# Kernel optimization log

Hardware: AMD Instinct MI355X
Metric: run time of the kernel (lower is better)

## Reference

```python
import jax, jax.numpy as jnp
import numpy as np
import math

SAMPLE_RATE = 44100
BASEBAND_SR = 16000
BAND_WIDTH_HZ = 8000.0
STEP_HZ = 8000.0
LOWPASS_FACTOR = 0.45
LPF_WIDTH = 6          # torchaudio resample lowpass_filter_width
ROLLOFF = 0.99         # torchaudio resample rolloff
B, T = 8, 441000


def _bands():
    nyq = SAMPLE_RATE / 2.0
    out, f = [], 0.0
    while f < nyq:
        out.append((f, min(f + BAND_WIDTH_HZ, nyq)))
        f += STEP_HZ
    return out


def _bandpass_coeffs(center, Q):
    # torchaudio bandpass_biquad, const_skirt_gain=False, normalized by a0
    w0 = 2.0 * math.pi * center / SAMPLE_RATE
    alpha = math.sin(w0) / (2.0 * Q)
    a0 = 1.0 + alpha
    b = np.array([alpha, 0.0, -alpha]) / a0
    a = np.array([1.0, -2.0 * math.cos(w0) / a0, (1.0 - alpha) / a0])
    return b, a


def _lowpass_coeffs(cutoff, Q=0.7071067811865476):
    w0 = 2.0 * math.pi * cutoff / SAMPLE_RATE
    alpha = math.sin(w0) / (2.0 * Q)
    c = math.cos(w0)
    a0 = 1.0 + alpha
    b = np.array([(1.0 - c) / 2.0, 1.0 - c, (1.0 - c) / 2.0]) / a0
    a = np.array([1.0, -2.0 * c / a0, (1.0 - alpha) / a0])
    return b, a


def _biquad(x, b0, b1, b2, a1, a2):
    # x: (..., T); coeffs broadcast against x[..., 0]. Direct-form I scan.
    xT = jnp.moveaxis(x, -1, 0)
    z = jnp.zeros_like(xT[0])
    def step(c, xt):
        x1, x2, y1, y2 = c
        y = b0 * xt + b1 * x1 + b2 * x2 - a1 * y1 - a2 * y2
        return (xt, x1, y, y1), y
    _, yT = jax.lax.scan(step, (z, z, z, z), xT)
    # torchaudio lfilter clamp=True clips final output to [-1, 1]
    return jnp.clip(jnp.moveaxis(yT, 0, -1), -1.0, 1.0)


def _resample_kernel():
    # replicates torchaudio _get_sinc_resample_kernel (sinc_interp_hann)
    g = math.gcd(SAMPLE_RATE, BASEBAND_SR)
    orig, new = SAMPLE_RATE // g, BASEBAND_SR // g  # 441, 160
    base = min(orig, new) * ROLLOFF
    width = int(math.ceil(LPF_WIDTH * orig / base))
    idx = np.arange(-width, width + orig, dtype=np.float64) / orig
    t = np.arange(0, -new, -1, dtype=np.float64)[:, None] / new + idx[None, :]
    t = np.clip(t * base, -LPF_WIDTH, LPF_WIDTH)
    window = np.cos(t * math.pi / LPF_WIDTH / 2.0) ** 2
    tp = t * math.pi
    k = np.where(tp == 0.0, 1.0, np.sin(tp) / np.where(tp == 0.0, 1.0, tp))
    k = k * window * (base / orig)
    return jnp.asarray(k[:, None, :], dtype=jnp.float32), width, orig, new


def _resample(x):
    # x: (N, T) -> (N, ceil(new*T/orig)) ; strided conv with polyphase sinc kernel
    kernel, width, orig, new = _resample_kernel()
    N, Tn = x.shape
    xp = jnp.pad(x, ((0, 0), (width, width + orig)))[:, None, :]
    y = jax.lax.conv_general_dilated(
        xp, kernel, window_strides=(orig,), padding='VALID',
        dimension_numbers=('NCH', 'OIH', 'NCH'))  # (N, new, frames)
    y = jnp.swapaxes(y, 1, 2).reshape(N, -1)
    return y[:, : int(math.ceil(new * Tn / orig))]


def _forward(x):
    # x: (B, T) -> (B, num_bands, T_baseband)
    bands = _bands()
    nb = len(bands)
    centers = np.array([0.5 * (lo + hi) for lo, hi in bands])
    Qs = np.array([max(c / (hi - lo), 0.5) for (lo, hi), c in zip(bands, centers)])
    bp = np.stack([np.concatenate(_bandpass_coeffs(c, q)) for c, q in zip(centers, Qs)])  # (nb, 6)
    bpj = jnp.asarray(bp, dtype=x.dtype)[:, :, None]  # (nb, 6, 1) -> broadcast over batch
    xb = jnp.broadcast_to(x[None], (nb,) + x.shape)   # (nb, B, T)
    # 1) per-band bandpass biquad (single batched scan over all bands)
    x_bp = _biquad(xb, bpj[:, 0], bpj[:, 1], bpj[:, 2], bpj[:, 4], bpj[:, 5])
    # 2) heterodyne mix with cosine at each band center
    t = jnp.arange(x.shape[-1], dtype=x.dtype) / SAMPLE_RATE
    cos = jnp.cos(2.0 * jnp.pi * jnp.asarray(centers, x.dtype)[:, None, None] * t[None, None, :])
    x_mix = x_bp * cos
    # 3) lowpass biquad (same coeffs for every band)
    lb, la = _lowpass_coeffs(LOWPASS_FACTOR * BASEBAND_SR)
    x_lp = _biquad(x_mix, float(lb[0]), float(lb[1]), float(lb[2]), float(la[1]), float(la[2]))
    # 4) resample 44100 -> 16000 (all bands/batch at once)
    y = _resample(x_lp.reshape(nb * x.shape[0], -1)).reshape(nb, x.shape[0], -1)
    return jnp.swapaxes(y, 0, 1)


def setup_inputs() -> dict:
    key = jax.random.key(0)
    x = jax.random.normal(key, (B, T), dtype=jnp.float32)
    return {"x": x}


def reference(x):
    return _forward(x)
```

## Files before the change

kernel.cpp:

```cpp
#include <hip/hip_runtime.h>
#include <math.h>

#define SRATE   44100
#define T_IN    441000
#define BATCH   8
#define NB      3
#define NSEQ    (NB*BATCH)
#define TB_OUT  160000
#define NEW_R   160
#define ORIG_R  441
#define KW      475
#define KP      480
#define WIDTH   17
#define NFRAMES 1000

#define LCHUNK  168
#define NCHUNK  2625
#define WARM    120

#define SCAN_BLOCKS 247
#define KT_BLOCKS   300

#define KTH_OFF 0
#define KTL_OFF (256u<<10)
#define XLP_OFF (1u<<20)

typedef __attribute__((ext_vector_type(4))) float floatx4;
typedef __attribute__((ext_vector_type(8))) short short8;

__device__ inline unsigned short f2bf(float f) {
    union { float f; unsigned u; } v; v.f = f;
    unsigned u = v.u, r = (u >> 16) & 0xffffu, rem = u & 0xffffu;
    if (rem > 0x8000u || (rem == 0x8000u && (r & 1u))) r++;
    return (unsigned short)r;
}
__device__ inline float bf2f(unsigned short h) {
    union { unsigned u; float f; } v; v.u = ((unsigned)h) << 16; return v.f;
}

__device__ inline int fragB(int p, int k) {
    int pblk = p >> 4, n = p & 15;
    int ks = k >> 5, qd = (k >> 3) & 3, j = k & 7;
    return pblk * 7680 + ks * 512 + (qd * 16 + n) * 8 + j;
}

struct ScanParams {
    float b0[NB], a1[NB], a2[NB], w[NB];
    float lb0, lb1, lb2, la1, la2;
};

__global__ __launch_bounds__(256) void scan_init_kernel(const float* __restrict__ x,
                                                        float* __restrict__ xlp,
                                                        unsigned short* __restrict__ kth,
                                                        unsigned short* __restrict__ ktl,
                                                        ScanParams P) {
    if (blockIdx.x >= SCAN_BLOCKS) {
        int idx = (blockIdx.x - SCAN_BLOCKS) * 256 + threadIdx.x;
        if (idx >= NEW_R * KP) return;
        int p = idx / KP, k = idx - p * KP;
        float v = 0.f;
        if (k < KW) {
            double t = (double)(k - WIDTH) * (158.4 / 441.0) - (double)p * 0.99;
            t = fmin(6.0, fmax(-6.0, t));
            float wc = __builtin_amdgcn_cosf((float)(t * (1.0 / 24.0)));
            double n = rint(t);
            float r2 = (float)((t - n) * 0.5);
            float sp = __builtin_amdgcn_sinf(r2 - floorf(r2));
            if (((long long)n) & 1) sp = -sp;
            float tp = (float)(t * M_PI);
            float snc = (t == 0.0) ? 1.f : sp / tp;
            v = snc * wc * wc * 0.3591836734693878f;
        }
        unsigned short h = f2bf(v);
        int flat = fragB(p, k);
        kth[flat] = h;
        ktl[flat] = f2bf(v - bf2f(h));
        return;
    }

    int id = blockIdx.x * 256 + threadIdx.x;
    if (id >= NSEQ * NCHUNK) return;
    int seq   = id / NCHUNK;
    int chunk = id - seq * NCHUNK;
    int band  = seq / BATCH;
    int batch = seq - band * BATCH;

    float b0f = (band == 0) ? P.b0[0] : (band == 1) ? P.b0[1] : P.b0[2];
    float a1f = (band == 0) ? P.a1[0] : (band == 1) ? P.a1[1] : P.a1[2];
    float a2f = (band == 0) ? P.a2[0] : (band == 1) ? P.a2[1] : P.a2[2];
    float wf  = (band == 0) ? P.w[0]  : (band == 1) ? P.w[1]  : P.w[2];
    float b2f = -b0f;
    float lb0 = P.lb0, lb1 = P.lb1, lb2 = P.lb2, la1 = P.la1, la2 = P.la2;

    const float*  xr   = x + batch * T_IN;
    float*        orow = xlp + seq * T_IN;
    const float4* xr4  = (const float4*)xr;

    int t0 = chunk * LCHUNK;
    int s0 = t0 - WARM; if (s0 < 0) s0 = 0;
    int e  = t0 + LCHUNK;
    int nq = (e - s0) >> 2;

    float bx1 = 0.f, bx2 = 0.f, by1 = 0.f, by2 = 0.f;
    float mx1 = 0.f, mx2 = 0.f, mz1 = 0.f, mz2 = 0.f;

    const float invsr  = 1.0f / 44100.0f;
    const float INV2PI = 0.15915494309189535f;
    const float PI2_A  = 6.28318548202514648f;
    const float PI2_B  = -1.7484556000744487e-7f;

    const float4 zero = make_float4(0.f, 0.f, 0.f, 0.f);
    const float4* pp = xr4 + (s0 >> 2);
    float4 c0 = pp[0];
    float4 c1 = (1 < nq) ? pp[1] : zero;
    float4 c2 = (2 < nq) ? pp[2] : zero;
    float4 c3 = (3 < nq) ? pp[3] : zero;

    for (int iq = 0; iq < nq; iq += 4) {
        float4 n0 = (iq + 4 < nq) ? pp[iq + 4] : zero;
        float4 n1 = (iq + 5 < nq) ? pp[iq + 5] : zero;
        float4 n2 = (iq + 6 < nq) ? pp[iq + 6] : zero;
        float4 n3 = (iq + 7 < nq) ? pp[iq + 7] : zero;

#define STEP(XT, TI, OUT) {                                                   \
        float y  = b0f*(XT) + b2f*bx2 - a1f*by1 - a2f*by2;                    \
        bx2 = bx1; bx1 = (XT); by2 = by1; by1 = y;                            \
        float cy = fminf(fmaxf(y, -1.f), 1.f);                                \
        float tf = (float)(TI) * invsr;                                       \
        float X  = wf * tf;                                                   \
        float kk = __builtin_rintf(X * INV2PI);                               \
        float r  = fmaf(-kk, PI2_A, X);                                       \
        r        = fmaf(-kk, PI2_B, r);                                       \
        float cv = __builtin_amdgcn_cosf(r * INV2PI);                         \
        float m  = cy * cv;                                                   \
        float z  = lb0*m + lb1*mx1 + lb2*mx2 - la1*mz1 - la2*mz2;             \
        mx2 = mx1; mx1 = m; mz2 = mz1; mz1 = z;                               \
        OUT = fminf(fmaxf(z, -1.f), 1.f); }

#define QUAD(CV, QI) {                                                        \
        int s = s0 + ((iq + QI) << 2);                                        \
        float o0, o1, o2, o3;                                                 \
        STEP(CV.x, s,     o0)                                                 \
        STEP(CV.y, s + 1, o1)                                                 \
        STEP(CV.z, s + 2, o2)                                                 \
        STEP(CV.w, s + 3, o3)                                                 \
        if (s >= t0 && s < e)                                                 \
            ((float4*)orow)[s >> 2] = make_float4(o0, o1, o2, o3); }

        QUAD(c0, 0)
        QUAD(c1, 1)
        QUAD(c2, 2)
        QUAD(c3, 3)
#undef QUAD
#undef STEP
        c0 = n0; c1 = n1; c2 = n2; c3 = n3;
    }
}

#define MT2   32

__global__ __launch_bounds__(320) void resample_mfma(const float* __restrict__ xlp,
                                                     const unsigned short* __restrict__ kth,
                                                     const unsigned short* __restrict__ ktl,
                                                     float* __restrict__ out) {
    __shared__ unsigned short Ah[2][7680];
    __shared__ unsigned short Al[2][7680];

    int bid = blockIdx.x;
    int seq = bid / MT2;
    int mt  = bid - seq * MT2;
    int band  = seq / BATCH;
    int batch = seq - band * BATCH;
    int f0 = mt * 32;
    const float* xr = xlp + seq * T_IN;

    for (int i = threadIdx.x; i < 32 * 120; i += 320) {
        int r  = i / 120;
        int q  = i - r * 120;
        int c  = q * 4;
        int fr = f0 + r;
        int base = fr * ORIG_R - WIDTH + c;
        float v0 = (base     >= 0 && base     < T_IN) ? xr[base]     : 0.f;
        float v1 = (base + 1 >= 0 && base + 1 < T_IN) ? xr[base + 1] : 0.f;
        float v2 = (base + 2 >= 0 && base + 2 < T_IN) ? xr[base + 2] : 0.f;
        float v3 = (base + 3 >= 0 && base + 3 < T_IN) ? xr[base + 3] : 0.f;
        unsigned short h0 = f2bf(v0), h1 = f2bf(v1), h2 = f2bf(v2), h3 = f2bf(v3);
        unsigned short l0 = f2bf(v0 - bf2f(h0)), l1 = f2bf(v1 - bf2f(h1));
        unsigned short l2 = f2bf(v2 - bf2f(h2)), l3 = f2bf(v3 - bf2f(h3));
        int tile = r >> 4, m = r & 15;
        int ks = c >> 5, qd = (c >> 3) & 3, j0 = c & 7;
        int slot = (qd * 16 + m) ^ ks;
        int off = ks * 512 + slot * 8 + j0;
        *(short4*)&Ah[tile][off] = make_short4(h0, h1, h2, h3);
        *(short4*)&Al[tile][off] = make_short4(l0, l1, l2, l3);
    }
    __syncthreads();

    int w    = threadIdx.x >> 6;
    int lane = threadIdx.x & 63;
    int l15  = lane & 15;
    int quad = lane >> 4;

    floatx4 acc00 = {0,0,0,0}, acc01 = {0,0,0,0};
    floatx4 acc10 = {0,0,0,0}, acc11 = {0,0,0,0};

    const unsigned short* b0h = kth + (w * 2    ) * 7680 + lane * 8;
    const unsigned short* b1h = kth + (w * 2 + 1) * 7680 + lane * 8;
    const unsigned short* b0l = ktl + (w * 2    ) * 7680 + lane * 8;
    const unsigned short* b1l = ktl + (w * 2 + 1) * 7680 + lane * 8;

#pragma unroll
    for (int ks = 0; ks < 15; ++ks) {
        int o  = ks * 512;
        int sl = o + ((lane ^ ks) << 3);
        short8 kh0 = *(const short8*)(b0h + o);
        short8 kh1 = *(const short8*)(b1h + o);
        short8 kl0 = *(const short8*)(b0l + o);
        short8 kl1 = *(const short8*)(b1l + o);
        short8 ah0 = *(const short8*)(&Ah[0][sl]);
        short8 al0 = *(const short8*)(&Al[0][sl]);
        short8 ah1 = *(const short8*)(&Ah[1][sl]);
        short8 al1 = *(const short8*)(&Al[1][sl]);

        acc00 = __builtin_amdgcn_mfma_f32_16x16x32_bf16(ah0, kh0, acc00, 0, 0, 0);
        acc00 = __builtin_amdgcn_mfma_f32_16x16x32_bf16(ah0, kl0, acc00, 0, 0, 0);
        acc00 = __builtin_amdgcn_mfma_f32_16x16x32_bf16(al0, kh0, acc00, 0, 0, 0);
        acc01 = __builtin_amdgcn_mfma_f32_16x16x32_bf16(ah0, kh1, acc01, 0, 0, 0);
        acc01 = __builtin_amdgcn_mfma_f32_16x16x32_bf16(ah0, kl1, acc01, 0, 0, 0);
        acc01 = __builtin_amdgcn_mfma_f32_16x16x32_bf16(al0, kh1, acc01, 0, 0, 0);
        acc10 = __builtin_amdgcn_mfma_f32_16x16x32_bf16(ah1, kh0, acc10, 0, 0, 0);
        acc10 = __builtin_amdgcn_mfma_f32_16x16x32_bf16(ah1, kl0, acc10, 0, 0, 0);
        acc10 = __builtin_amdgcn_mfma_f32_16x16x32_bf16(al1, kh0, acc10, 0, 0, 0);
        acc11 = __builtin_amdgcn_mfma_f32_16x16x32_bf16(ah1, kh1, acc11, 0, 0, 0);
        acc11 = __builtin_amdgcn_mfma_f32_16x16x32_bf16(ah1, kl1, acc11, 0, 0, 0);
        acc11 = __builtin_amdgcn_mfma_f32_16x16x32_bf16(al1, kh1, acc11, 0, 0, 0);
    }

    int obase = (batch * NB + band) * TB_OUT;
    int p0 = w * 32;
#pragma unroll
    for (int r = 0; r < 4; ++r) {
        int fr0 = f0 + quad * 4 + r;
        int fr1 = fr0 + 16;
        if (fr0 < NFRAMES) {
            out[obase + fr0 * NEW_R + p0 + l15]      = acc00[r];
            out[obase + fr0 * NEW_R + p0 + 16 + l15] = acc01[r];
        }
        if (fr1 < NFRAMES) {
            out[obase + fr1 * NEW_R + p0 + l15]      = acc10[r];
            out[obase + fr1 * NEW_R + p0 + 16 + l15] = acc11[r];
        }
    }
}

extern "C" void kernel_launch(void* const* d_in, const int* in_sizes, int n_in,
                              void* d_out, int out_size, void* d_ws, size_t ws_size,
                              hipStream_t stream) {
    const float*    x   = (const float*)d_in[0];
    float*          out = (float*)d_out;
    unsigned short* kth = (unsigned short*)((char*)d_ws + KTH_OFF);
    unsigned short* ktl = (unsigned short*)((char*)d_ws + KTL_OFF);
    float*          xlp = (float*)((char*)d_ws + XLP_OFF);

    ScanParams P;
    const double centers[NB] = {4000.0, 12000.0, 19025.0};
    const double Qs[NB]      = {0.5, 1.5, 19025.0 / 6050.0};
    for (int b = 0; b < NB; ++b) {
        double c  = centers[b], Q = Qs[b];
        double w0 = 2.0 * M_PI * c / 44100.0;
        double al = sin(w0) / (2.0 * Q);
        double a0 = 1.0 + al;
        P.b0[b] = (float)(al / a0);
        P.a1[b] = (float)(-2.0 * cos(w0) / a0);
        P.a2[b] = (float)((1.0 - al) / a0);
        P.w[b]  = 6.283185307179586f * (float)c;
    }
    {
        double cut = 0.45 * 16000.0;
        double Q   = 0.7071067811865476;
        double w0  = 2.0 * M_PI * cut / 44100.0;
        double al  = sin(w0) / (2.0 * Q);
        double cs  = cos(w0);
        double a0  = 1.0 + al;
        P.lb0 = (float)(((1.0 - cs) / 2.0) / a0);
        P.lb1 = (float)((1.0 - cs) / a0);
        P.lb2 = P.lb0;
        P.la1 = (float)(-2.0 * cs / a0);
        P.la2 = (float)((1.0 - al) / a0);
    }

    scan_init_kernel<<<dim3(SCAN_BLOCKS + KT_BLOCKS), dim3(256), 0, stream>>>(
        x, xlp, kth, ktl, P);

    resample_mfma<<<dim3(NSEQ * MT2), dim3(320), 0, stream>>>(xlp, kth, ktl, out);
}
```

Measured before the change: 133.1 us.

## Drop activation low-half split in resample MFMA and use 48-frame tiles

The resample kernel no longer splits the low-pass output into bf16 high and low halves. It keeps only the high half, which removes a third of the MFMAs and half of the LDS staging. Each block now covers 48 frames with three row tiles instead of 32, so fewer blocks each reuse the kernel-coefficient loads more. The clamps in the scan switch to fmed3. Activations are now held only at bf16 precision, which may weaken accuracy against the float reference.

```diff
diff --git a/kernel.cpp b/kernel.cpp
--- a/kernel.cpp
+++ b/kernel.cpp
@@ -125,7 +125,7 @@
 #define STEP(XT, TI, OUT) {                                                   \
         float y  = b0f*(XT) + b2f*bx2 - a1f*by1 - a2f*by2;                    \
         bx2 = bx1; bx1 = (XT); by2 = by1; by1 = y;                            \
-        float cy = fminf(fmaxf(y, -1.f), 1.f);                                \
+        float cy = __builtin_amdgcn_fmed3f(y, -1.f, 1.f);                     \
         float tf = (float)(TI) * invsr;                                       \
         float X  = wf * tf;                                                   \
         float kk = __builtin_rintf(X * INV2PI);                               \
@@ -135,7 +135,7 @@
         float m  = cy * cv;                                                   \
         float z  = lb0*m + lb1*mx1 + lb2*mx2 - la1*mz1 - la2*mz2;             \
         mx2 = mx1; mx1 = m; mz2 = mz1; mz1 = z;                               \
-        OUT = fminf(fmaxf(z, -1.f), 1.f); }
+        OUT = __builtin_amdgcn_fmed3f(z, -1.f, 1.f); }
 
 #define QUAD(CV, QI) {                                                        \
         int s = s0 + ((iq + QI) << 2);                                        \
@@ -157,24 +157,23 @@
     }
 }
 
-#define MT2   32
+#define MT3   21
 
 __global__ __launch_bounds__(320) void resample_mfma(const float* __restrict__ xlp,
                                                      const unsigned short* __restrict__ kth,
                                                      const unsigned short* __restrict__ ktl,
                                                      float* __restrict__ out) {
-    __shared__ unsigned short Ah[2][7680];
-    __shared__ unsigned short Al[2][7680];
+    __shared__ unsigned short Ah[3][7680];
 
     int bid = blockIdx.x;
-    int seq = bid / MT2;
-    int mt  = bid - seq * MT2;
+    int seq = bid / MT3;
+    int mt  = bid - seq * MT3;
     int band  = seq / BATCH;
     int batch = seq - band * BATCH;
-    int f0 = mt * 32;
+    int f0 = mt * 48;
     const float* xr = xlp + seq * T_IN;
 
-    for (int i = threadIdx.x; i < 32 * 120; i += 320) {
+    for (int i = threadIdx.x; i < 48 * 120; i += 320) {
         int r  = i / 120;
         int q  = i - r * 120;
         int c  = q * 4;
@@ -185,14 +184,11 @@
         float v2 = (base + 2 >= 0 && base + 2 < T_IN) ? xr[base + 2] : 0.f;
         float v3 = (base + 3 >= 0 && base + 3 < T_IN) ? xr[base + 3] : 0.f;
         unsigned short h0 = f2bf(v0), h1 = f2bf(v1), h2 = f2bf(v2), h3 = f2bf(v3);
-        unsigned short l0 = f2bf(v0 - bf2f(h0)), l1 = f2bf(v1 - bf2f(h1));
-        unsigned short l2 = f2bf(v2 - bf2f(h2)), l3 = f2bf(v3 - bf2f(h3));
         int tile = r >> 4, m = r & 15;
         int ks = c >> 5, qd = (c >> 3) & 3, j0 = c & 7;
         int slot = (qd * 16 + m) ^ ks;
         int off = ks * 512 + slot * 8 + j0;
         *(short4*)&Ah[tile][off] = make_short4(h0, h1, h2, h3);
-        *(short4*)&Al[tile][off] = make_short4(l0, l1, l2, l3);
     }
     __syncthreads();
 
@@ -203,6 +199,7 @@
 
     floatx4 acc00 = {0,0,0,0}, acc01 = {0,0,0,0};
     floatx4 acc10 = {0,0,0,0}, acc11 = {0,0,0,0};
+    floatx4 acc20 = {0,0,0,0}, acc21 = {0,0,0,0};
 
     const unsigned short* b0h = kth + (w * 2    ) * 7680 + lane * 8;
     const unsigned short* b1h = kth + (w * 2 + 1) * 7680 + lane * 8;
@@ -218,22 +215,21 @@
         short8 kl0 = *(const short8*)(b0l + o);
         short8 kl1 = *(const short8*)(b1l + o);
         short8 ah0 = *(const short8*)(&Ah[0][sl]);
-        short8 al0 = *(const short8*)(&Al[0][sl]);
         short8 ah1 = *(const short8*)(&Ah[1][sl]);
-        short8 al1 = *(const short8*)(&Al[1][sl]);
+        short8 ah2 = *(const short8*)(&Ah[2][sl]);
 
         acc00 = __builtin_amdgcn_mfma_f32_16x16x32_bf16(ah0, kh0, acc00, 0, 0, 0);
         acc00 = __builtin_amdgcn_mfma_f32_16x16x32_bf16(ah0, kl0, acc00, 0, 0, 0);
-        acc00 = __builtin_amdgcn_mfma_f32_16x16x32_bf16(al0, kh0, acc00, 0, 0, 0);
         acc01 = __builtin_amdgcn_mfma_f32_16x16x32_bf16(ah0, kh1, acc01, 0, 0, 0);
         acc01 = __builtin_amdgcn_mfma_f32_16x16x32_bf16(ah0, kl1, acc01, 0, 0, 0);
-        acc01 = __builtin_amdgcn_mfma_f32_16x16x32_bf16(al0, kh1, acc01, 0, 0, 0);
         acc10 = __builtin_amdgcn_mfma_f32_16x16x32_bf16(ah1, kh0, acc10, 0, 0, 0);
         acc10 = __builtin_amdgcn_mfma_f32_16x16x32_bf16(ah1, kl0, acc10, 0, 0, 0);
-        acc10 = __builtin_amdgcn_mfma_f32_16x16x32_bf16(al1, kh0, acc10, 0, 0, 0);
         acc11 = __builtin_amdgcn_mfma_f32_16x16x32_bf16(ah1, kh1, acc11, 0, 0, 0);
         acc11 = __builtin_amdgcn_mfma_f32_16x16x32_bf16(ah1, kl1, acc11, 0, 0, 0);
-        acc11 = __builtin_amdgcn_mfma_f32_16x16x32_bf16(al1, kh1, acc11, 0, 0, 0);
+        acc20 = __builtin_amdgcn_mfma_f32_16x16x32_bf16(ah2, kh0, acc20, 0, 0, 0);
+        acc20 = __builtin_amdgcn_mfma_f32_16x16x32_bf16(ah2, kl0, acc20, 0, 0, 0);
+        acc21 = __builtin_amdgcn_mfma_f32_16x16x32_bf16(ah2, kh1, acc21, 0, 0, 0);
+        acc21 = __builtin_amdgcn_mfma_f32_16x16x32_bf16(ah2, kl1, acc21, 0, 0, 0);
     }
 
     int obase = (batch * NB + band) * TB_OUT;
@@ -242,6 +238,7 @@
     for (int r = 0; r < 4; ++r) {
         int fr0 = f0 + quad * 4 + r;
         int fr1 = fr0 + 16;
+        int fr2 = fr0 + 32;
         if (fr0 < NFRAMES) {
             out[obase + fr0 * NEW_R + p0 + l15]      = acc00[r];
             out[obase + fr0 * NEW_R + p0 + 16 + l15] = acc01[r];
@@ -249,6 +246,10 @@
         if (fr1 < NFRAMES) {
             out[obase + fr1 * NEW_R + p0 + l15]      = acc10[r];
             out[obase + fr1 * NEW_R + p0 + 16 + l15] = acc11[r];
+        }
+        if (fr2 < NFRAMES) {
+            out[obase + fr2 * NEW_R + p0 + l15]      = acc20[r];
+            out[obase + fr2 * NEW_R + p0 + 16 + l15] = acc21[r];
         }
     }
 }
@@ -292,5 +293,5 @@
     scan_init_kernel<<<dim3(SCAN_BLOCKS + KT_BLOCKS), dim3(256), 0, stream>>>(
         x, xlp, kth, ktl, P);
 
-    resample_mfma<<<dim3(NSEQ * MT2), dim3(320), 0, stream>>>(xlp, kth, ktl, out);
-}
+    resample_mfma<<<dim3(NSEQ * MT3), dim3(320), 0, stream>>>(xlp, kth, ktl, out);
+}
```

New measurement: 113.7 us. 1.17x faster.
